# Kernel tuning notes

Hardware: AMD Instinct MI355X
Metric: run time of the kernel (lower is better)

The kernel has to match this reference:

```python
import jax, jax.numpy as jnp
import numpy as np

B, T, C, H = 4, 2048, 1024, 16
D = C // H  # head_dim = 64


def setup_inputs() -> dict:
    key = jax.random.key(0)
    k1, k2, k3 = jax.random.split(key, 3)
    x = jax.random.normal(k1, (B, T, C), dtype=jnp.float32)
    # torch Linear init ~ U(-1/sqrt(fan_in), 1/sqrt(fan_in)); scaled normal is fine for a baseline
    w_qkv = jax.random.normal(k2, (C, 3 * C), dtype=jnp.float32) * (1.0 / np.sqrt(C))
    w_proj = jax.random.normal(k3, (C, C), dtype=jnp.float32) * (1.0 / np.sqrt(C))
    return {"x": x, "w_qkv": w_qkv, "w_proj": w_proj}


def reference(x, w_qkv, w_proj):
    Bb, Tt, Cc = x.shape
    qkv = x @ w_qkv                                   # [B,T,3C]
    q, k, v = jnp.split(qkv, 3, axis=-1)
    # [B,T,C] -> [B,H,T,D]
    q = q.reshape(Bb, Tt, H, D).transpose(0, 2, 1, 3)
    k = k.reshape(Bb, Tt, H, D).transpose(0, 2, 1, 3)
    v = v.reshape(Bb, Tt, H, D).transpose(0, 2, 1, 3)
    scale = 1.0 / np.sqrt(D).astype(np.float32)
    logits = jnp.einsum("bhqd,bhkd->bhqk", q, k) * scale  # [B,H,T,T]
    causal = jnp.tril(jnp.ones((Tt, Tt), dtype=bool))
    logits = jnp.where(causal, logits, jnp.finfo(logits.dtype).min)
    attn = jax.nn.softmax(logits, axis=-1)
    y = jnp.einsum("bhqk,bhkd->bhqd", attn, v)            # [B,H,T,D]
    y = y.transpose(0, 2, 1, 3).reshape(Bb, Tt, Cc)
    return y @ w_proj                                     # dropout p=0 (eval)
```

## Files before the change

### kernel.cpp

```cpp
#include <hip/hip_runtime.h>
#include <hip/hip_bf16.h>
#include <stdint.h>

typedef unsigned short u16;
typedef __attribute__((ext_vector_type(4))) float f32x4;
typedef __attribute__((ext_vector_type(16))) float f32x16;
typedef __attribute__((ext_vector_type(8))) __bf16 bf16x8;
typedef __attribute__((ext_vector_type(2))) unsigned int u32x2;

__device__ __forceinline__ u16 f2bf(float f) {
  union { float f; uint32_t u; } x; x.f = f;
  const uint32_t u = x.u;
  return (u16)((u + 0x7fffu + ((u >> 16) & 1u)) >> 16);
}

#define QSCALE 0.1803368801111244f

__global__ void cvt_f32_bf16(const float* __restrict__ in, u16* __restrict__ out,
                             int n) {
  const int i = (blockIdx.x * blockDim.x + threadIdx.x) * 4;
  if (i < n) {
    const float4 v = *(const float4*)(in + i);
    ushort4 o;
    o.x = f2bf(v.x); o.y = f2bf(v.y); o.z = f2bf(v.z); o.w = f2bf(v.w);
    *(ushort4*)(out + i) = o;
  }
}

__global__ void transpose_cvt(const float* __restrict__ in, u16* __restrict__ out,
                              int R, int Cc) {
  __shared__ u16 tile[64][66];
  const int tx = threadIdx.x, ty = threadIdx.y;
  const int c0 = blockIdx.x * 64, r0 = blockIdx.y * 64;
#pragma unroll
  for (int i = 0; i < 4; ++i)
    tile[ty + i * 16][tx] = f2bf(in[(size_t)(r0 + ty + i * 16) * Cc + c0 + tx]);
  __syncthreads();
#pragma unroll
  for (int i = 0; i < 4; ++i)
    out[(size_t)(c0 + ty + i * 16) * R + r0 + tx] = tile[tx][ty + i * 16];
}

__global__ void transpose_v(const u16* __restrict__ V, u16* __restrict__ VT) {
  __shared__ u16 tile[64][66];
  const int tx = threadIdx.x, ty = threadIdx.y;
  const int r0 = blockIdx.x * 64;
  const size_t ho = (size_t)blockIdx.y * 2048 * 64;
  const u16* in = V + ho;
  u16* out = VT + ho;
#pragma unroll
  for (int i = 0; i < 4; ++i)
    tile[ty + i * 16][tx] = in[(size_t)(r0 + ty + i * 16) * 64 + tx];
  __syncthreads();
#pragma unroll
  for (int i = 0; i < 4; ++i)
    out[(size_t)(ty + i * 16) * 2048 + r0 + tx] = tile[tx][ty + i * 16];
}

template <int MODE>
__global__ __launch_bounds__(512, 2) void gemm8p(
    const u16* __restrict__ A, const u16* __restrict__ BT,
    u16* __restrict__ Qo, u16* __restrict__ Ko, u16* __restrict__ Vo,
    float* __restrict__ out, int Nout, int K) {
  __shared__ u16 LA[2][128 * 64];
  __shared__ u16 LB[2][2][128 * 64];
  const int tid = threadIdx.x, wid = tid >> 6, lane = tid & 63;
  const int wm = wid >> 2, wn = wid & 3;
  const int l15 = lane & 15, l4 = lane >> 4;
  const int bn = blockIdx.x, bm = blockIdx.y;

  const u16* Atile = A + (size_t)bm * 128 * K;
  const u16* Btile = BT + (size_t)bn * 256 * K;

  f32x4 acc[4][4] = {};
  bf16x8 aF[4][2], bF[4][2];
  const int cb = wid * 64 + lane;

#define SB8() __builtin_amdgcn_sched_barrier(0)
#define BAR8() { SB8(); __builtin_amdgcn_s_barrier(); SB8(); }
#define VW4() { SB8(); asm volatile("s_waitcnt vmcnt(4)" ::: "memory"); SB8(); }
#define STGU(dst, srcbase) { \
    const u16* s0_ = (srcbase); \
    _Pragma("unroll") for (int j_ = 0; j_ < 2; ++j_) { \
      const int c_ = j_ * 512 + cb; \
      const int r_ = c_ >> 3; \
      const int g_ = (c_ & 7) ^ (r_ & 7); \
      __builtin_amdgcn_global_load_lds( \
          (const __attribute__((address_space(1))) uint32_t*)(s0_ + (size_t)r_ * K + g_ * 8), \
          (__attribute__((address_space(3))) uint32_t*)(&(dst)[(j_ * 512 + wid * 64) * 8]), 16, 0, 0); \
    } }
#define STG_A(d, kt) STGU(LA[d], Atile + (size_t)(kt) * 64)
#define STG_B(d, h, kt) STGU(LB[d][h], Btile + (size_t)(h) * 128 * K + (size_t)(kt) * 64)
#define LD_A(d) { \
    _Pragma("unroll") for (int m_ = 0; m_ < 4; ++m_) \
    _Pragma("unroll") for (int k_ = 0; k_ < 2; ++k_) \
      aF[m_][k_] = *(const bf16x8*)&LA[d][(wm * 64 + m_ * 16 + l15) * 64 + (((k_ * 4 + l4) ^ (l15 & 7)) * 8)]; }
#define LD_B(d, nbase) { \
    _Pragma("unroll") for (int n_ = 0; n_ < 2; ++n_) \
    _Pragma("unroll") for (int k_ = 0; k_ < 2; ++k_) \
      bF[(nbase) + n_][k_] = *(const bf16x8*)&LB[d][wn >> 1][((wn & 1) * 64 + ((nbase) + n_) * 16 + l15) * 64 + (((k_ * 4 + l4) ^ (l15 & 7)) * 8)]; }
#define MQ(MS, NS) { __builtin_amdgcn_s_setprio(1); \
    _Pragma("unroll") for (int m_ = 0; m_ < 2; ++m_) \
    _Pragma("unroll") for (int n_ = 0; n_ < 2; ++n_) \
    _Pragma("unroll") for (int kk_ = 0; kk_ < 2; ++kk_) \
      acc[(MS) * 2 + m_][(NS) * 2 + n_] = __builtin_amdgcn_mfma_f32_16x16x32_bf16( \
          aF[(MS) * 2 + m_][kk_], bF[(NS) * 2 + n_][kk_], acc[(MS) * 2 + m_][(NS) * 2 + n_], 0, 0, 0); \
    __builtin_amdgcn_s_setprio(0); }

  STG_A(0, 0); STG_B(0, 0, 0); STG_B(0, 1, 0);
  STG_A(1, 1); STG_B(1, 0, 1);
  VW4();
  BAR8();

  const int nkt = K >> 6;
  for (int it = 0; it < nkt / 2; ++it) {
    const int t1 = 2 * it + 1;
    const int t2 = (2 * it + 2 < nkt) ? 2 * it + 2 : nkt - 1;
    const int t3 = (2 * it + 3 < nkt) ? 2 * it + 3 : nkt - 1;
    LD_A(0); LD_B(0, 0);
    STG_B(1, 1, t1);
    BAR8(); MQ(0, 0); BAR8();
    STG_A(0, t2);
    BAR8(); MQ(1, 0); BAR8();
    LD_B(0, 2);
    BAR8(); MQ(0, 1); BAR8();
    STG_B(0, 0, t2);
    VW4();
    BAR8(); MQ(1, 1); BAR8();
    LD_A(1); LD_B(1, 0);
    STG_B(0, 1, t2);
    BAR8(); MQ(0, 0); BAR8();
    STG_A(1, t3);
    BAR8(); MQ(1, 0); BAR8();
    LD_B(1, 2);
    BAR8(); MQ(0, 1); BAR8();
    STG_B(1, 0, t3);
    VW4();
    BAR8(); MQ(1, 1); BAR8();
  }
  asm volatile("s_waitcnt vmcnt(0)" ::: "memory");

  const int row0 = bm * 128 + wm * 64;
  const int col0 = bn * 256 + wn * 64;
#pragma unroll
  for (int m = 0; m < 4; ++m) {
#pragma unroll
    for (int n = 0; n < 4; ++n) {
#pragma unroll
      for (int jj = 0; jj < 4; ++jj) {
        const int row = row0 + m * 16 + l4 * 4 + jj;
        const int col = col0 + n * 16 + l15;
        if (MODE == 1) {
          const int sec = col >> 10, c = col & 1023;
          const int h = c >> 6, d = c & 63;
          const int b = row >> 11, t = row & 2047;
          float av = acc[m][n][jj];
          if (sec == 0) av *= QSCALE;
          u16* dst = (sec == 0) ? Qo : (sec == 1) ? Ko : Vo;
          dst[(((size_t)(b * 16 + h)) * 2048 + t) * 64 + d] = f2bf(av);
        } else {
          out[(size_t)row * Nout + col] = acc[m][n][jj];
        }
      }
    }
  }
#undef SB8
#undef BAR8
#undef VW4
#undef STGU
#undef STG_A
#undef STG_B
#undef LD_A
#undef LD_B
#undef MQ
}

__global__ __launch_bounds__(256, 4) void attn_fwd(const u16* __restrict__ Qp,
                                                   const u16* __restrict__ Kp,
                                                   const u16* __restrict__ VTp,
                                                   u16* __restrict__ Y) {
  constexpr int DP = 72;
  constexpr float THR = 11.0f;
  __shared__ u16 Ks[2][64 * DP];
  __shared__ u16 Vt[2][64 * DP];

  const int xorm = (int)((0x0A050F00u >> ((blockIdx.y >> 4) * 8)) & 15u);
  const int qt = (int)blockIdx.x ^ xorm;
  const int bh = blockIdx.y;
  const int b = bh >> 4, h = bh & 15;
  const int tid = threadIdx.x, lane = tid & 63;
  const int wid = tid >> 6;
  const int l31 = lane & 31, hb = lane >> 5;

  const size_t head_off = (size_t)bh * 2048 * 64;
  const u16* Kh = Kp + head_off;
  const u16* VTh = VTp + head_off;

  const int qg = qt * 128 + wid * 32 + l31;
  const u16* Qrow = Qp + head_off + (size_t)qg * 64;

  bf16x8 qf[4];
#pragma unroll
  for (int d = 0; d < 4; ++d)
    qf[d] = *(const bf16x8*)(Qrow + d * 16 + hb * 8);

  bf16x8 ones;
#pragma unroll
  for (int i = 0; i < 8; ++i) ones[i] = (__bf16)1.0f;

  float m_ = -1e30f;
  f32x16 oacc[2] = {};
  f32x16 lacc = {};

  const int sr = tid >> 3;
  const int sc = (tid & 7) * 8;

  bf16x8 kreg[2], vreg[2];
  auto kvload = [&](int kt) {
#pragma unroll
    for (int it = 0; it < 2; ++it) {
      const int r = sr + it * 32;
      kreg[it] = *(const bf16x8*)(Kh + (size_t)(kt * 64 + r) * 64 + sc);
      vreg[it] = *(const bf16x8*)(VTh + (size_t)r * 2048 + kt * 64 + sc);
    }
  };
  auto kvwrite = [&](int buf) {
#pragma unroll
    for (int it = 0; it < 2; ++it) {
      const int r = sr + it * 32;
      *(bf16x8*)&Ks[buf][r * DP + sc] = kreg[it];
      *(bf16x8*)&Vt[buf][r * DP + sc] = vreg[it];
    }
  };

  kvload(0);
  kvwrite(0);
  __syncthreads();

  const int nt = 2 * qt + 2;
  for (int kt = 0; kt < nt; ++kt) {
    const int cur = kt & 1;
    const bool havenext = (kt + 1 < nt);
    if (havenext) kvload(kt + 1);

    const bool diag = (kt >= 2 * qt);

#pragma unroll
    for (int kb2 = 0; kb2 < 2; ++kb2) {
      f32x16 s = {};
      __builtin_amdgcn_s_setprio(1);
#pragma unroll
      for (int d = 0; d < 4; ++d) {
        const bf16x8 kf = *(const bf16x8*)&Ks[cur][(kb2 * 32 + l31) * DP + d * 16 + hb * 8];
        s = __builtin_amdgcn_mfma_f32_32x32x16_bf16(kf, qf[d], s, 0, 0, 0);
      }
      __builtin_amdgcn_s_setprio(0);

      if (diag) {
        const int kbase = kt * 64 + kb2 * 32 + hb * 4;
#pragma unroll
        for (int r = 0; r < 16; ++r) {
          const int koff = (r & 3) + 8 * (r >> 2);
          if (kbase + koff > qg) s[r] = -1e30f;
        }
      }

      float pmax = s[0];
#pragma unroll
      for (int r = 1; r < 16; ++r) pmax = fmaxf(pmax, s[r]);
      if (!__all(pmax - m_ <= THR)) {
        const float fm = fmaxf(pmax, __shfl_xor(pmax, 32));
        const float mnew = fmaxf(m_, fm);
        const float alpha = __builtin_exp2f(m_ - mnew);
        m_ = mnew;
#pragma unroll
        for (int r = 0; r < 16; ++r) lacc[r] *= alpha;
#pragma unroll
        for (int nb = 0; nb < 2; ++nb)
#pragma unroll
          for (int r = 0; r < 16; ++r) oacc[nb][r] *= alpha;
      }
#pragma unroll
      for (int r = 0; r < 16; ++r)
        s[r] = __builtin_exp2f(s[r] - m_);

      bf16x8 pb[2];
#pragma unroll
      for (int st = 0; st < 2; ++st) {
        uint32_t x0, x1, y0, y1;
        asm("v_cvt_pk_bf16_f32 %0, %1, %2" : "=v"(x0) : "v"(s[8 * st + 0]), "v"(s[8 * st + 1]));
        asm("v_cvt_pk_bf16_f32 %0, %1, %2" : "=v"(x1) : "v"(s[8 * st + 2]), "v"(s[8 * st + 3]));
        asm("v_cvt_pk_bf16_f32 %0, %1, %2" : "=v"(y0) : "v"(s[8 * st + 4]), "v"(s[8 * st + 5]));
        asm("v_cvt_pk_bf16_f32 %0, %1, %2" : "=v"(y1) : "v"(s[8 * st + 6]), "v"(s[8 * st + 7]));
        const u32x2 r0 = __builtin_amdgcn_permlane32_swap(x0, y0, false, false);
        const u32x2 r1 = __builtin_amdgcn_permlane32_swap(x1, y1, false, false);
        union { uint32_t w[4]; bf16x8 v; } u;
        u.w[0] = r0[0]; u.w[1] = r1[0]; u.w[2] = r0[1]; u.w[3] = r1[1];
        pb[st] = u.v;
      }

      __builtin_amdgcn_s_setprio(1);
#pragma unroll
      for (int st = 0; st < 2; ++st) {
        lacc = __builtin_amdgcn_mfma_f32_32x32x16_bf16(ones, pb[st], lacc, 0, 0, 0);
#pragma unroll
        for (int nb = 0; nb < 2; ++nb) {
          const bf16x8 vf = *(const bf16x8*)&Vt[cur][(nb * 32 + l31) * DP + kb2 * 32 + st * 16 + hb * 8];
          oacc[nb] = __builtin_amdgcn_mfma_f32_32x32x16_bf16(vf, pb[st], oacc[nb], 0, 0, 0);
        }
      }
      __builtin_amdgcn_s_setprio(0);
    }

    if (havenext) kvwrite(cur ^ 1);
    __syncthreads();
  }

  const float inv = 1.0f / lacc[0];
  u16* Yrow = Y + ((size_t)b * 2048 + qg) * 1024 + h * 64;
#pragma unroll
  for (int nb = 0; nb < 2; ++nb) {
#pragma unroll
    for (int g = 0; g < 4; ++g) {
      ushort4 o;
      o.x = f2bf(oacc[nb][4 * g + 0] * inv);
      o.y = f2bf(oacc[nb][4 * g + 1] * inv);
      o.z = f2bf(oacc[nb][4 * g + 2] * inv);
      o.w = f2bf(oacc[nb][4 * g + 3] * inv);
      *(ushort4*)(Yrow + nb * 32 + g * 8 + hb * 4) = o;
    }
  }
}

extern "C" void kernel_launch(void* const* d_in, const int* in_sizes, int n_in,
                              void* d_out, int out_size, void* d_ws,
                              size_t ws_size, hipStream_t stream) {
  const float* x = (const float*)d_in[0];
  const float* w_qkv = (const float*)d_in[1];
  const float* w_proj = (const float*)d_in[2];
  float* out = (float*)d_out;

  char* ws = (char*)d_ws;
  u16* xb = (u16*)ws;
  u16* VTw = (u16*)ws;
  u16* wqkvT = (u16*)(ws + 16777216);
  u16* wprojT = (u16*)(ws + 23068672);
  u16* Qw = (u16*)(ws + 25165824);
  u16* Kw = (u16*)(ws + 41943040);
  u16* Vw = (u16*)(ws + 58720256);
  u16* Yw = (u16*)(ws + 75497472);
  if (ws_size < 92274688) return;

  cvt_f32_bf16<<<dim3(8192), dim3(256), 0, stream>>>(x, xb, 8388608);

  dim3 tb(64, 16);
  transpose_cvt<<<dim3(48, 16), tb, 0, stream>>>(w_qkv, wqkvT, 1024, 3072);
  transpose_cvt<<<dim3(16, 16), tb, 0, stream>>>(w_proj, wprojT, 1024, 1024);

  gemm8p<1><<<dim3(12, 64), dim3(512), 0, stream>>>(
      xb, wqkvT, Qw, Kw, Vw, (float*)nullptr, 0, 1024);

  transpose_v<<<dim3(32, 64), tb, 0, stream>>>(Vw, VTw);

  attn_fwd<<<dim3(16, 64), dim3(256), 0, stream>>>(Qw, Kw, VTw, Yw);

  gemm8p<0><<<dim3(4, 64), dim3(512), 0, stream>>>(
      Yw, wprojT, (u16*)nullptr, (u16*)nullptr, (u16*)nullptr, out, 1024, 1024);
}
```

Measured before the change: 195.1 us.

## Split causal attention KV range across two blocks and merge partials in a combine kernel

Each query tile's key range is split into two halves handled by separate blocks, which doubles the grid and balances the causal workload. Each block writes a normalized partial output plus its running max and row sum. A new combine kernel rescales and merges the two partials into the head-interleaved layout. LDS double buffering is replaced by a single buffer with two barriers per tile. The trade-off is extra global traffic and a kernel launch for the combine step, plus lower latency hiding in the main loop.

Result: slower. 212.3 us (+8.8%).

```diff
diff --git a/kernel.cpp b/kernel.cpp
--- a/kernel.cpp
+++ b/kernel.cpp
@@ -12,6 +12,9 @@
   union { float f; uint32_t u; } x; x.f = f;
   const uint32_t u = x.u;
   return (u16)((u + 0x7fffu + ((u >> 16) & 1u)) >> 16);
+}
+__device__ __forceinline__ float bf2f(u16 v) {
+  union { uint32_t u; float f; } x; x.u = ((uint32_t)v) << 16; return x.f;
 }
 
 #define QSCALE 0.1803368801111244f
@@ -175,19 +178,21 @@
 #undef MQ
 }
 
-__global__ __launch_bounds__(256, 4) void attn_fwd(const u16* __restrict__ Qp,
-                                                   const u16* __restrict__ Kp,
-                                                   const u16* __restrict__ VTp,
-                                                   u16* __restrict__ Y) {
+__global__ __launch_bounds__(256, 4) void attn_fwd(
+    const u16* __restrict__ Qp, const u16* __restrict__ Kp,
+    const u16* __restrict__ VTp, u16* __restrict__ OpL,
+    u16* __restrict__ OpH, float2* __restrict__ ml) {
   constexpr int DP = 72;
   constexpr float THR = 11.0f;
-  __shared__ u16 Ks[2][64 * DP];
-  __shared__ u16 Vt[2][64 * DP];
-
-  const int xorm = (int)((0x0A050F00u >> ((blockIdx.y >> 4) * 8)) & 15u);
-  const int qt = (int)blockIdx.x ^ xorm;
+  __shared__ u16 Ks[64 * DP];
+  __shared__ u16 Vt[64 * DP];
+
+  const uint64_t PACK = 0ULL | 30ULL << 5 | 10ULL << 10 | 20ULL << 15 |
+                        6ULL << 20 | 24ULL << 25 | 12ULL << 30 | 18ULL << 35;
+  const int mask5 = (int)((PACK >> (5 * ((blockIdx.y >> 3) & 7))) & 31u);
+  const int wxr = (int)blockIdx.x ^ mask5;
+  const int qt = wxr >> 1, half = wxr & 1;
   const int bh = blockIdx.y;
-  const int b = bh >> 4, h = bh & 15;
   const int tid = threadIdx.x, lane = tid & 63;
   const int wid = tid >> 6;
   const int l31 = lane & 31, hb = lane >> 5;
@@ -224,24 +229,24 @@
       vreg[it] = *(const bf16x8*)(VTh + (size_t)r * 2048 + kt * 64 + sc);
     }
   };
-  auto kvwrite = [&](int buf) {
+  auto kvwrite = [&]() {
 #pragma unroll
     for (int it = 0; it < 2; ++it) {
       const int r = sr + it * 32;
-      *(bf16x8*)&Ks[buf][r * DP + sc] = kreg[it];
-      *(bf16x8*)&Vt[buf][r * DP + sc] = vreg[it];
+      *(bf16x8*)&Ks[r * DP + sc] = kreg[it];
+      *(bf16x8*)&Vt[r * DP + sc] = vreg[it];
     }
   };
 
-  kvload(0);
-  kvwrite(0);
-  __syncthreads();
-
-  const int nt = 2 * qt + 2;
-  for (int kt = 0; kt < nt; ++kt) {
-    const int cur = kt & 1;
-    const bool havenext = (kt + 1 < nt);
-    if (havenext) kvload(kt + 1);
+  const int k0 = half ? (qt + 1) : 0;
+  const int k1 = half ? (2 * qt + 2) : (qt + 1);
+
+  kvload(k0);
+  for (int kt = k0; kt < k1; ++kt) {
+    __syncthreads();
+    kvwrite();
+    if (kt + 1 < k1) kvload(kt + 1);
+    __syncthreads();
 
     const bool diag = (kt >= 2 * qt);
 
@@ -251,7 +256,7 @@
       __builtin_amdgcn_s_setprio(1);
 #pragma unroll
       for (int d = 0; d < 4; ++d) {
-        const bf16x8 kf = *(const bf16x8*)&Ks[cur][(kb2 * 32 + l31) * DP + d * 16 + hb * 8];
+        const bf16x8 kf = *(const bf16x8*)&Ks[(kb2 * 32 + l31) * DP + d * 16 + hb * 8];
         s = __builtin_amdgcn_mfma_f32_32x32x16_bf16(kf, qf[d], s, 0, 0, 0);
       }
       __builtin_amdgcn_s_setprio(0);
@@ -305,31 +310,67 @@
         lacc = __builtin_amdgcn_mfma_f32_32x32x16_bf16(ones, pb[st], lacc, 0, 0, 0);
 #pragma unroll
         for (int nb = 0; nb < 2; ++nb) {
-          const bf16x8 vf = *(const bf16x8*)&Vt[cur][(nb * 32 + l31) * DP + kb2 * 32 + st * 16 + hb * 8];
+          const bf16x8 vf = *(const bf16x8*)&Vt[(nb * 32 + l31) * DP + kb2 * 32 + st * 16 + hb * 8];
           oacc[nb] = __builtin_amdgcn_mfma_f32_32x32x16_bf16(vf, pb[st], oacc[nb], 0, 0, 0);
         }
       }
       __builtin_amdgcn_s_setprio(0);
     }
-
-    if (havenext) kvwrite(cur ^ 1);
-    __syncthreads();
-  }
-
+  }
+
+  const size_t g = (size_t)bh * 2048 + qg;
   const float inv = 1.0f / lacc[0];
-  u16* Yrow = Y + ((size_t)b * 2048 + qg) * 1024 + h * 64;
+  u16* Orow = (half ? OpH : OpL) + g * 64;
 #pragma unroll
   for (int nb = 0; nb < 2; ++nb) {
 #pragma unroll
-    for (int g = 0; g < 4; ++g) {
+    for (int gg = 0; gg < 4; ++gg) {
       ushort4 o;
-      o.x = f2bf(oacc[nb][4 * g + 0] * inv);
-      o.y = f2bf(oacc[nb][4 * g + 1] * inv);
-      o.z = f2bf(oacc[nb][4 * g + 2] * inv);
-      o.w = f2bf(oacc[nb][4 * g + 3] * inv);
-      *(ushort4*)(Yrow + nb * 32 + g * 8 + hb * 4) = o;
+      o.x = f2bf(oacc[nb][4 * gg + 0] * inv);
+      o.y = f2bf(oacc[nb][4 * gg + 1] * inv);
+      o.z = f2bf(oacc[nb][4 * gg + 2] * inv);
+      o.w = f2bf(oacc[nb][4 * gg + 3] * inv);
+      *(ushort4*)(Orow + nb * 32 + gg * 8 + hb * 4) = o;
     }
   }
+  if (hb == 0) {
+    float2 v; v.x = m_; v.y = lacc[0];
+    ml[(size_t)half * 131072 + g] = v;
+  }
+}
+
+__global__ __launch_bounds__(256) void attn_combine(
+    const u16* __restrict__ OpL, const u16* __restrict__ OpH,
+    const float2* __restrict__ ml, u16* __restrict__ Yf) {
+  const int tid = threadIdx.x;
+  const size_t g = (size_t)blockIdx.x * 64 + (tid >> 2);
+  const int c = (tid & 3) * 16;
+  const float2 a = ml[g], bq = ml[131072 + g];
+  const float m = fmaxf(a.x, bq.x);
+  const float w1 = __builtin_exp2f(a.x - m) * a.y;
+  const float w2 = __builtin_exp2f(bq.x - m) * bq.y;
+  const float den = 1.0f / (w1 + w2);
+  const float c1 = w1 * den, c2 = w2 * den;
+
+  union { ushort4 s[2]; bf16x8 v; } l0, l1, h0, h1, o0, o1;
+  l0.v = *(const bf16x8*)(OpL + g * 64 + c);
+  l1.v = *(const bf16x8*)(OpL + g * 64 + c + 8);
+  h0.v = *(const bf16x8*)(OpH + g * 64 + c);
+  h1.v = *(const bf16x8*)(OpH + g * 64 + c + 8);
+  const u16* lu = (const u16*)&l0; const u16* hu = (const u16*)&h0;
+  u16* ou = (u16*)&o0;
+#pragma unroll
+  for (int i = 0; i < 8; ++i) ou[i] = f2bf(c1 * bf2f(lu[i]) + c2 * bf2f(hu[i]));
+  const u16* lu1 = (const u16*)&l1; const u16* hu1 = (const u16*)&h1;
+  u16* ou1 = (u16*)&o1;
+#pragma unroll
+  for (int i = 0; i < 8; ++i) ou1[i] = f2bf(c1 * bf2f(lu1[i]) + c2 * bf2f(hu1[i]));
+
+  const int bh = (int)(g >> 11), t = (int)(g & 2047);
+  const int b = bh >> 4, h = bh & 15;
+  u16* dst = Yf + ((size_t)(b * 2048 + t)) * 1024 + h * 64 + c;
+  *(bf16x8*)dst = o0.v;
+  *(bf16x8*)(dst + 8) = o1.v;
 }
 
 extern "C" void kernel_launch(void* const* d_in, const int* in_sizes, int n_in,
@@ -343,12 +384,16 @@
   char* ws = (char*)d_ws;
   u16* xb = (u16*)ws;
   u16* VTw = (u16*)ws;
+  u16* Yf = (u16*)ws;
   u16* wqkvT = (u16*)(ws + 16777216);
+  float2* mlw = (float2*)(ws + 16777216);
   u16* wprojT = (u16*)(ws + 23068672);
   u16* Qw = (u16*)(ws + 25165824);
   u16* Kw = (u16*)(ws + 41943040);
   u16* Vw = (u16*)(ws + 58720256);
+  u16* OpH = (u16*)(ws + 58720256);
   u16* Yw = (u16*)(ws + 75497472);
+  u16* OpL = (u16*)(ws + 75497472);
   if (ws_size < 92274688) return;
 
   cvt_f32_bf16<<<dim3(8192), dim3(256), 0, stream>>>(x, xb, 8388608);
@@ -362,8 +407,10 @@
 
   transpose_v<<<dim3(32, 64), tb, 0, stream>>>(Vw, VTw);
 
-  attn_fwd<<<dim3(16, 64), dim3(256), 0, stream>>>(Qw, Kw, VTw, Yw);
+  attn_fwd<<<dim3(32, 64), dim3(256), 0, stream>>>(Qw, Kw, VTw, OpL, OpH, mlw);
+
+  attn_combine<<<dim3(2048), dim3(256), 0, stream>>>(OpL, OpH, mlw, Yf);
 
   gemm8p<0><<<dim3(4, 64), dim3(512), 0, stream>>>(
-      Yw, wprojT, (u16*)nullptr, (u16*)nullptr, (u16*)nullptr, out, 1024, 1024);
-}
+      Yf, wprojT, (u16*)nullptr, (u16*)nullptr, (u16*)nullptr, out, 1024, 1024);
+}
```
